# Kernel optimization log

Measured on AMD Instinct MI355X. Metric: run time of the kernel, lower is better.

The kernel has to match this reference:

```python
import jax, jax.numpy as jnp
import numpy as np
import math

B, S, FDIM, D_MODEL, N_SCALES = 8, 2048, 64, 512, 5

def _layer_norm(h, g, b, eps=1e-5):
    mu = h.mean(-1, keepdims=True)
    var = h.var(-1, keepdims=True)
    return (h - mu) * jax.lax.rsqrt(var + eps) * g + b

def setup_inputs() -> dict:
    key = jax.random.key(0)
    ks = jax.random.split(key, 12)
    sc = lambda fan_in: 1.0 / np.sqrt(fan_in)
    inp = {
        'x': jax.random.normal(ks[0], (B, S, FDIM), dtype=jnp.float32),
        # relative_positional_encoding: Linear(3, d_model)
        'w_rel': jax.random.uniform(ks[1], (D_MODEL, 3), minval=-sc(3), maxval=sc(3), dtype=jnp.float32),
        'b_rel': jnp.zeros((D_MODEL,), jnp.float32),
        # event_encoding_projection: Linear(feature_dim, d_model)
        'w_proj': jax.random.uniform(ks[2], (D_MODEL, FDIM), minval=-sc(FDIM), maxval=sc(FDIM), dtype=jnp.float32),
        'b_proj': jnp.zeros((D_MODEL,), jnp.float32),
        'g1': jnp.ones((D_MODEL,), jnp.float32), 'bt1': jnp.zeros((D_MODEL,), jnp.float32),
        'g2': jnp.ones((D_MODEL,), jnp.float32), 'bt2': jnp.zeros((D_MODEL,), jnp.float32),
        'alpha': jnp.asarray(0.5, jnp.float32),
        'sigma_w': jnp.ones((1,), jnp.float32),
        'wq': jax.random.uniform(ks[3], (FDIM, FDIM), minval=-sc(FDIM), maxval=sc(FDIM), dtype=jnp.float32),
        'bq': jnp.zeros((FDIM,), jnp.float32),
        'wk': jax.random.uniform(ks[4], (FDIM, FDIM), minval=-sc(FDIM), maxval=sc(FDIM), dtype=jnp.float32),
        'bk': jnp.zeros((FDIM,), jnp.float32),
        'scale_w': jax.nn.softplus(jax.random.normal(ks[5], (N_SCALES,), dtype=jnp.float32)),
    }
    return inp

def reference(x, w_rel, b_rel, w_proj, b_proj, g1, bt1, g2, bt2, alpha, sigma_w, wq, bq, wk, bk, scale_w):
    bsz, seq_len, fdim = x.shape
    # distances / energies are the first two physical feature channels
    distances = x[:, :, 0]
    energies = x[:, :, 1]
    dd_list, de_list, wd_list = [], [], []
    for scale in range(1, N_SCALES + 1):  # static small loop (clamp(5,3,15).round()=5)
        dd = distances[:, :-scale] - distances[:, scale:]
        de = energies[:, :-scale] - energies[:, scale:]
        wd = scale_w[scale - 1] * jnp.exp(-jnp.abs(dd) / (2.0 ** scale))
        pad = ((0, 0), (scale, 0))
        dd_list.append(jnp.pad(dd, pad))
        de_list.append(jnp.pad(de, pad))
        wd_list.append(jnp.pad(wd, pad))
    delta_distances = jnp.stack(dd_list, axis=-1)   # [B,S,n_scales]
    delta_energies = jnp.stack(de_list, axis=-1)
    weighted_distances = jnp.stack(wd_list, axis=-1)
    rel = jnp.stack([delta_distances, delta_energies, weighted_distances], axis=-1)  # [B,S,n_scales,3]
    rel_enc = (jnp.einsum('bsnt,dt->bsnd', rel, w_rel) + b_rel).sum(axis=2)  # [B,S,D]
    rel_enc = _layer_norm(rel_enc, g1, bt1)

    # hybrid similarity
    x_norm = x / jnp.maximum(jnp.linalg.norm(x, axis=-1, keepdims=True), 1e-12)
    cos_sim = (jnp.einsum('bsd,btd->bst', x_norm, x_norm) + 1.0) / 2.0
    # pairwise euclidean distance via gram trick (avoids B*S*S*d intermediate)
    sq = jnp.sum(x * x, axis=-1)                                  # [B,S]
    d2 = sq[:, :, None] + sq[:, None, :] - 2.0 * jnp.einsum('bsd,btd->bst', x, x)
    d2 = jnp.maximum(d2, 0.0)
    euclid = jnp.where(d2 > 0, jnp.sqrt(jnp.maximum(d2, 1e-12)), 0.0)
    mean_dist = euclid.mean()
    std_dist = jnp.std(euclid, ddof=1)
    dev = euclid - mean_dist
    euclid = jnp.where(jnp.abs(dev) > 2 * std_dist, jnp.sign(dev) * (2 * std_dist) + mean_dist, euclid)
    euclid = (euclid - euclid.min()) / (euclid.max() - euclid.min() + 1e-6)
    a = jax.nn.sigmoid(alpha)
    hybrid = a * cos_sim + (1 - a) * (1 - euclid)

    sigma = jax.nn.softplus(sigma_w) + 0.001          # [1]
    q = jnp.einsum('bsf,gf->bsg', x, wq) + bq
    k = jnp.einsum('bsf,gf->bsg', x, wk) + bk
    scores = jnp.einsum('bsg,btg->bst', q, k) / math.sqrt(fdim)
    weights = jax.nn.softmax(scores, axis=-1)
    E = weights * jnp.exp(-hybrid / (2.0 * sigma[0] ** 2))
    pe_event = jnp.einsum('bst,btf->bsf', E, x)
    pe_proj = jnp.einsum('bsf,df->bsd', pe_event, w_proj) + b_proj
    pe_proj = _layer_norm(pe_proj, g2, bt2)
    return rel_enc + pe_proj
```

## Files before the change

kernel.cpp:

```cpp
#include <hip/hip_runtime.h>
#include <math.h>

#define B_ 8
#define S_ 2048
#define F_ 64
#define D_ 512
#define NS_ 5
#define BS_ (B_*S_)
#define NTILE_ 528
#define NPART_ (NTILE_*B_)

typedef unsigned short u16;
typedef __attribute__((ext_vector_type(8))) short short8;
typedef __attribute__((ext_vector_type(4))) float f32x4;

#define WS_SQ    0
#define WS_REL   (BS_)
#define WS_PE    (4*BS_)
#define WS_STATS (68*BS_)
#define US_BASE_FLOATS (68*BS_ + 16)
#define US_XB 0
#define US_QB (BS_*64)
#define US_KB (2*BS_*64)
#define US_XT (3*BS_*64)

#define MFMA16(a,b,c) __builtin_amdgcn_mfma_f32_16x16x32_bf16(a,b,c,0,0,0)

__device__ __forceinline__ u16 f2bf(float f){
  unsigned u = __float_as_uint(f);
  return (u16)((u + 0x7FFFu + ((u>>16)&1u)) >> 16);
}
__device__ __forceinline__ int swz_phys(int row, int c){ return row*64 + (((c ^ (row & 15))) << 2); }

__global__ __launch_bounds__(256) void k1_prep(
    const float* __restrict__ x, const float* __restrict__ wq, const float* __restrict__ bq,
    const float* __restrict__ wk, const float* __restrict__ bk,
    const float* __restrict__ scale_w, float* __restrict__ ws, u16* __restrict__ usb)
{
  __shared__ __align__(16) float xl[16*68];
  __shared__ __align__(16) float wql[4096];
  __shared__ __align__(16) float wkl[4096];
  int tid = threadIdx.x, lane = tid & 63, wv = tid >> 6;
  int row0 = blockIdx.x * 16;
  {
    int r = tid >> 4, c = tid & 15;
    *(float4*)(xl + r*68 + c*4) = *(const float4*)(x + (size_t)(row0 + r)*F_ + c*4);
  }
  for (int i = 0; i < 4; ++i){
    int idx = tid + i*256;
    int g = idx >> 4, c = idx & 15;
    float4 v = *(const float4*)(wq + g*F_ + c*4);
    int pb = swz_phys(g, c);
    wql[pb]=v.x; wql[pb+1]=v.y; wql[pb+2]=v.z; wql[pb+3]=v.w;
    float4 u = *(const float4*)(wk + g*F_ + c*4);
    wkl[pb]=u.x; wkl[pb+1]=u.y; wkl[pb+2]=u.z; wkl[pb+3]=u.w;
  }
  __syncthreads();
  int g = lane;
  int swl = g & 15;
  float qa[4], ka[4];
  #pragma unroll
  for (int j=0;j<4;++j){ qa[j]=bq[g]; ka[j]=bk[g]; }
  #pragma unroll
  for (int c=0;c<16;++c){
    float4 wqv = *(const float4*)(wql + g*64 + ((c ^ swl)<<2));
    float4 wkv = *(const float4*)(wkl + g*64 + ((c ^ swl)<<2));
    #pragma unroll
    for (int j=0;j<4;++j){
      float4 xv = *(const float4*)(xl + (wv*4+j)*68 + c*4);
      qa[j] += xv.x*wqv.x + xv.y*wqv.y + xv.z*wqv.z + xv.w*wqv.w;
      ka[j] += xv.x*wkv.x + xv.y*wkv.y + xv.z*wkv.z + xv.w*wkv.w;
    }
  }
  #pragma unroll
  for (int j=0;j<4;++j){
    int rg = row0 + wv*4 + j;
    usb[US_QB + (size_t)rg*64 + g] = f2bf(qa[j]);
    usb[US_KB + (size_t)rg*64 + g] = f2bf(ka[j]);
  }
  #pragma unroll
  for (int j=0;j<4;++j){
    int r = wv*4 + j;
    float v = xl[r*68 + lane];
    float s = v*v;
    for (int o=32;o;o>>=1) s += __shfl_xor(s, o, 64);
    if (lane == 0) ws[WS_SQ + row0 + r] = s;
  }
  #pragma unroll
  for (int j=0;j<4;++j){
    int r = wv*4 + j;
    int rg = row0 + r;
    int b = rg >> 11, s_loc = rg & (S_-1);
    float d0 = xl[r*68 + 0], e0 = xl[r*68 + 1];
    float dd = 0.f, de = 0.f, wd = 0.f;
    int n = lane + 1;
    if (lane < NS_ && s_loc >= n){
      const float* xp = x + ((size_t)(b*S_ + s_loc - n))*F_;
      float dp_ = xp[0], ep = xp[1];
      dd = dp_ - d0;
      de = ep - e0;
      wd = scale_w[lane] * __expf(-fabsf(dd) * (1.0f/(float)(1<<n)));
    }
    for (int o=4;o;o>>=1){
      dd += __shfl_down(dd, o, 64);
      de += __shfl_down(de, o, 64);
      wd += __shfl_down(wd, o, 64);
    }
    if (lane == 0){
      ws[WS_REL + rg*3+0] = dd;
      ws[WS_REL + rg*3+1] = de;
      ws[WS_REL + rg*3+2] = wd;
    }
  }
  {
    int r = tid >> 4, cb = (tid & 15)*4;
    unsigned w0 = (unsigned)f2bf(xl[r*68+cb])   | ((unsigned)f2bf(xl[r*68+cb+1])<<16);
    unsigned w1 = (unsigned)f2bf(xl[r*68+cb+2]) | ((unsigned)f2bf(xl[r*68+cb+3])<<16);
    uint2 pk; pk.x = w0; pk.y = w1;
    *(uint2*)(usb + US_XB + (size_t)(row0+r)*64 + cb) = pk;
  }
  {
    int f = tid & 63, rg4 = (tid >> 6)*4;
    unsigned wa = (unsigned)f2bf(xl[(rg4+0)*68+f]) | ((unsigned)f2bf(xl[(rg4+1)*68+f])<<16);
    unsigned wb = (unsigned)f2bf(xl[(rg4+2)*68+f]) | ((unsigned)f2bf(xl[(rg4+3)*68+f])<<16);
    uint2 pk; pk.x = wa; pk.y = wb;
    int bb = row0 >> 11;
    int tloc = (row0 & (S_-1)) + rg4;
    *(uint2*)(usb + US_XT + (size_t)bb*64*2048 + (size_t)f*2048 + tloc) = pk;
  }
}

__global__ __launch_bounds__(256) void k2_stats(const u16* __restrict__ us, float* __restrict__ ws)
{
  __shared__ __align__(16) u16 Xls[4096];
  __shared__ float sqs_l[64], sqt_l[64];
  __shared__ float rsum[4], rss[4], rmn[4], rmx[4];
  int tid = threadIdx.x, lane = tid & 63, wv = tid >> 6;
  int lg = lane >> 4, lc = lane & 15;
  int b = blockIdx.y;
  int rem = blockIdx.x, i = 0;
  while (rem >= 32 - i){ rem -= 32 - i; ++i; }
  int j = i + rem;
  int s0 = i*64, t0 = j*64;
  size_t rb = (size_t)b * S_;
  const u16* xb = us + US_XB;
  #pragma unroll
  for (int p2=0;p2<2;++p2){
    int slot = tid + p2*256;
    int row = slot>>3, pc = slot&7, lcn = pc ^ (row&7);
    ((short8*)Xls)[slot] = *(const short8*)(xb + (rb + t0 + row)*64 + lcn*8);
  }
  if (tid < 64) sqs_l[tid] = ws[WS_SQ + rb + s0 + tid];
  else if (tid < 128) sqt_l[tid-64] = ws[WS_SQ + rb + t0 + (tid-64)];
  short8 a0 = *(const short8*)(xb + (rb + s0 + wv*16 + lc)*64 + lg*8);
  short8 a1 = *(const short8*)(xb + (rb + s0 + wv*16 + lc)*64 + 32 + lg*8);
  __syncthreads();
  f32x4 acc[4];
  #pragma unroll
  for (int t=0;t<4;++t){ acc[t][0]=0.f; acc[t][1]=0.f; acc[t][2]=0.f; acc[t][3]=0.f; }
  #pragma unroll
  for (int ts=0; ts<4; ++ts){
    int rowb = ts*16 + lc;
    int sw = rowb & 7;
    short8 b0 = *(const short8*)(Xls + rowb*64 + ((lg ^ sw)<<3));
    short8 b1 = *(const short8*)(Xls + rowb*64 + (((4+lg) ^ sw)<<3));
    acc[ts] = MFMA16(a0, b0, acc[ts]);
    acc[ts] = MFMA16(a1, b1, acc[ts]);
  }
  float sq_s[4];
  #pragma unroll
  for (int r=0;r<4;++r) sq_s[r] = sqs_l[wv*16 + lg*4 + r];
  float lsum=0.f, lss=0.f, lmn=3.4e38f, lmx=-3.4e38f;
  #pragma unroll
  for (int ts=0; ts<4; ++ts){
    float sqt = sqt_l[ts*16 + lc];
    #pragma unroll
    for (int r=0;r<4;++r){
      float gg = acc[ts][r];
      float d2 = sq_s[r] + sqt - 2.f*gg;
      d2 = fmaxf(d2, 0.f);
      float eu = d2 > 0.f ? sqrtf(d2) : 0.f;
      lsum += eu; lss += eu*eu;
      lmn = fminf(lmn, eu); lmx = fmaxf(lmx, eu);
    }
  }
  for (int o=32;o;o>>=1){
    lsum += __shfl_xor(lsum, o, 64);
    lss  += __shfl_xor(lss, o, 64);
    lmn = fminf(lmn, __shfl_xor(lmn, o, 64));
    lmx = fmaxf(lmx, __shfl_xor(lmx, o, 64));
  }
  if (lane == 0){ rsum[wv]=lsum; rss[wv]=lss; rmn[wv]=lmn; rmx[wv]=lmx; }
  __syncthreads();
  if (tid == 0){
    float bs=0.f, bss=0.f, bmn=3.4e38f, bmx=-3.4e38f;
    for (int w2=0;w2<4;++w2){ bs+=rsum[w2]; bss+=rss[w2]; bmn=fminf(bmn,rmn[w2]); bmx=fmaxf(bmx,rmx[w2]); }
    float wgt = (i==j) ? 1.f : 2.f;
    float* part = ws + WS_PE;
    int bid = blockIdx.y * NTILE_ + blockIdx.x;
    part[bid]           = bs*wgt;
    part[NPART_ + bid]  = bss*wgt;
    part[2*NPART_ + bid]= bmn;
    part[3*NPART_ + bid]= bmx;
  }
}

__global__ __launch_bounds__(256) void k3_fin(const float* __restrict__ alpha,
                                              const float* __restrict__ sigma_w, float* ws){
  __shared__ double ssm[256], sss[256];
  __shared__ float smn[256], smx[256];
  int tid = threadIdx.x;
  const float* part = ws + WS_PE;
  double s = 0.0, ss = 0.0;
  float mn = 3.4e38f, mx = -3.4e38f;
  for (int i2 = tid; i2 < NPART_; i2 += 256){
    s  += (double)part[i2];
    ss += (double)part[NPART_ + i2];
    mn = fminf(mn, part[2*NPART_ + i2]);
    mx = fmaxf(mx, part[3*NPART_ + i2]);
  }
  ssm[tid]=s; sss[tid]=ss; smn[tid]=mn; smx[tid]=mx;
  __syncthreads();
  for (int st = 128; st; st >>= 1){
    if (tid < st){
      ssm[tid] += ssm[tid+st];
      sss[tid] += sss[tid+st];
      smn[tid] = fminf(smn[tid], smn[tid+st]);
      smx[tid] = fmaxf(smx[tid], smx[tid+st]);
    }
    __syncthreads();
  }
  if (tid == 0){
    double N = (double)B_*S_*S_;
    double sum = ssm[0], sumsq = sss[0];
    double mean = sum/N;
    double var  = (sumsq - sum*sum/N) / (N - 1.0);
    float stdv = (float)sqrt(fmax(var, 0.0));
    float m = (float)mean;
    float lo = m - 2.f*stdv, hi = m + 2.f*stdv;
    float cmn = fminf(fmaxf(smn[0], lo), hi);
    float cmx = fminf(fmaxf(smx[0], lo), hi);
    float invr = 1.f/(cmx - cmn + 1e-6f);
    float a = 1.f/(1.f + expf(-alpha[0]));
    float swv = sigma_w[0];
    float sp = (swv > 20.f) ? swv : log1pf(expf(swv));
    float sg = sp + 0.001f;
    float efac = -0.5f/(sg*sg);
    float* p = ws + WS_STATS + 8;
    p[0]=lo; p[1]=hi; p[2]=cmn; p[3]=invr; p[4]=a; p[5]=1.f-a; p[6]=efac;
  }
}

__global__ __launch_bounds__(512) void k4_flash(const u16* __restrict__ us, float* __restrict__ ws)
{
  __shared__ __align__(16) u16 SMEM[16384];
  __shared__ float sqt_l[64], invt_l[64];
  __shared__ float zb[4][2][16];
  u16* Kls  = SMEM;
  u16* Xls  = SMEM + 4096;
  u16* XTls = SMEM + 8192;
  u16* elp  = SMEM + 12288;
  int tid = threadIdx.x, lane = tid & 63, wv = tid >> 6;
  int lg = lane >> 4, lc = lane & 15;
  int ssub = wv >> 1, th = wv & 1;
  int b = blockIdx.y;
  size_t rb = (size_t)b * S_;
  int s0 = blockIdx.x * 64;
  const u16* xb = us + US_XB;
  const u16* qb = us + US_QB;
  const u16* kb = us + US_KB;
  const u16* xt = us + US_XT + (size_t)b*64*2048;
  int srow = s0 + ssub*16 + lc;
  short8 qf0 = *(const short8*)(qb + (rb+srow)*64 + lg*8);
  short8 qf1 = *(const short8*)(qb + (rb+srow)*64 + 32 + lg*8);
  short8 xf0 = *(const short8*)(xb + (rb+srow)*64 + lg*8);
  short8 xf1 = *(const short8*)(xb + (rb+srow)*64 + 32 + lg*8);
  float sq_s[4], inv_s[4];
  #pragma unroll
  for (int r=0;r<4;++r){
    float s = ws[WS_SQ + rb + s0 + ssub*16 + lg*4 + r];
    sq_s[r] = s; inv_s[r] = 1.f / fmaxf(sqrtf(s), 1e-12f);
  }
  const float* prm = ws + WS_STATS + 8;
  float lo=prm[0], hi=prm[1], cmn=prm[2], invr=prm[3], a=prm[4], oma=prm[5], efac=prm[6];
  f32x4 pe[4];
  #pragma unroll
  for (int t=0;t<4;++t){ pe[t][0]=0.f; pe[t][1]=0.f; pe[t][2]=0.f; pe[t][3]=0.f; }
  float zrun[4];
  #pragma unroll
  for (int r=0;r<4;++r) zrun[r]=0.f;

  for (int t0 = 0; t0 < S_; t0 += 64){
    {
      int slot = tid;
      int row = slot>>3, pc = slot&7, lcn = pc ^ (row&7);
      ((short8*)Kls)[slot]  = *(const short8*)(kb + (rb + t0 + row)*64 + lcn*8);
      ((short8*)Xls)[slot]  = *(const short8*)(xb + (rb + t0 + row)*64 + lcn*8);
      ((short8*)XTls)[slot] = *(const short8*)(xt + (size_t)row*2048 + t0 + lcn*8);
    }
    if (tid < 64){
      float s = ws[WS_SQ + rb + t0 + tid];
      sqt_l[tid] = s;
      invt_l[tid] = 1.f / fmaxf(sqrtf(s), 1e-12f);
    }
    __syncthreads();
    f32x4 ga[2], sa[2];
    #pragma unroll
    for (int t=0;t<2;++t){ ga[t][0]=0.f; ga[t][1]=0.f; ga[t][2]=0.f; ga[t][3]=0.f;
                           sa[t][0]=0.f; sa[t][1]=0.f; sa[t][2]=0.f; sa[t][3]=0.f; }
    #pragma unroll
    for (int ts=0; ts<2; ++ts){
      int rowb = (2*th+ts)*16 + lc;
      int sw = rowb & 7;
      short8 bk0 = *(const short8*)(Kls + rowb*64 + ((lg ^ sw)<<3));
      short8 bx0 = *(const short8*)(Xls + rowb*64 + ((lg ^ sw)<<3));
      sa[ts] = MFMA16(qf0, bk0, sa[ts]);
      ga[ts] = MFMA16(xf0, bx0, ga[ts]);
      short8 bk1 = *(const short8*)(Kls + rowb*64 + (((4+lg) ^ sw)<<3));
      short8 bx1 = *(const short8*)(Xls + rowb*64 + (((4+lg) ^ sw)<<3));
      sa[ts] = MFMA16(qf1, bk1, sa[ts]);
      ga[ts] = MFMA16(xf1, bx1, ga[ts]);
    }
    #pragma unroll
    for (int ts=0; ts<2; ++ts){
      int col = (2*th+ts)*16 + lc;
      float sqt = sqt_l[col], invt = invt_l[col];
      #pragma unroll
      for (int r=0;r<4;++r){
        float gg = ga[ts][r];
        float cosv = (gg*inv_s[r]*invt + 1.f)*0.5f;
        float d2 = sq_s[r] + sqt - 2.f*gg;
        d2 = fmaxf(d2, 0.f);
        float eu = d2 > 0.f ? sqrtf(d2) : 0.f;
        eu = fminf(fmaxf(eu, lo), hi);
        float en = (eu - cmn)*invr;
        float hyb = a*cosv + oma*(1.f - en);
        float H = __expf(hyb*efac);
        float p = __expf(__builtin_fmaf(sa[ts][r], 0.125f, -8.f));
        zrun[r] += p;
        int rowl = lg*4 + r;
        int phys = rowl*64 + ((((col>>3) ^ (rowl&7)))<<3) + (col&7);
        elp[ssub*1024 + phys] = f2bf(p*H);
      }
    }
    {
      int swA = lc & 7;
      short8 Ae = *(const short8*)(elp + ssub*1024 + lc*64 + (((4*th + lg) ^ swA)<<3));
      #pragma unroll
      for (int fs=0; fs<4; ++fs){
        int rowf = fs*16 + lc;
        short8 Bx = *(const short8*)(XTls + rowf*64 + (((4*th + lg) ^ (rowf&7))<<3));
        pe[fs] = MFMA16(Ae, Bx, pe[fs]);
      }
    }
    __syncthreads();
  }
  #pragma unroll
  for (int r=0;r<4;++r){
    float z = zrun[r];
    z += __shfl_xor(z, 1, 64);
    z += __shfl_xor(z, 2, 64);
    z += __shfl_xor(z, 4, 64);
    z += __shfl_xor(z, 8, 64);
    if (lc == r) zb[ssub][th][lg*4+r] = z;
  }
  __syncthreads();
  float* tmp = (float*)SMEM;
  if (th == 1){
    #pragma unroll
    for (int fs=0; fs<4; ++fs)
      #pragma unroll
      for (int r=0;r<4;++r)
        tmp[ssub*1024 + (lg*4+r)*64 + fs*16 + lc] = pe[fs][r];
  }
  __syncthreads();
  if (th == 0){
    float zi[4];
    #pragma unroll
    for (int r=0;r<4;++r) zi[r] = 1.f / (zb[ssub][0][lg*4+r] + zb[ssub][1][lg*4+r]);
    #pragma unroll
    for (int fs=0; fs<4; ++fs)
      #pragma unroll
      for (int r=0;r<4;++r){
        float v = pe[fs][r] + tmp[ssub*1024 + (lg*4+r)*64 + fs*16 + lc];
        ws[WS_PE + (rb + s0 + ssub*16 + lg*4 + r)*64 + fs*16 + lc] = v * zi[r];
      }
  }
}

__global__ __launch_bounds__(256) void kpe_conv(const float* __restrict__ pef, u16* __restrict__ usb){
  size_t i = ((size_t)blockIdx.x*256 + threadIdx.x)*4;
  float4 v = *(const float4*)(pef + i);
  uint2 pk;
  pk.x = (unsigned)f2bf(v.x) | ((unsigned)f2bf(v.y)<<16);
  pk.y = (unsigned)f2bf(v.z) | ((unsigned)f2bf(v.w)<<16);
  *(uint2*)(usb + US_QB + i) = pk;
}

__global__ __launch_bounds__(256) void kw_conv(const float* __restrict__ wp, u16* __restrict__ usb){
  int i = (blockIdx.x*256 + threadIdx.x)*4;
  float4 v = *(const float4*)(wp + i);
  uint2 pk;
  pk.x = (unsigned)f2bf(v.x) | ((unsigned)f2bf(v.y)<<16);
  pk.y = (unsigned)f2bf(v.z) | ((unsigned)f2bf(v.w)<<16);
  *(uint2*)(usb + US_KB + i) = pk;
}

__global__ __launch_bounds__(256) void k5_final(
    const float* __restrict__ w_rel, const float* __restrict__ b_rel,
    const float* __restrict__ b_proj,
    const float* __restrict__ g1, const float* __restrict__ bt1,
    const float* __restrict__ g2, const float* __restrict__ bt2,
    const float* __restrict__ ws, const u16* __restrict__ usb, float* __restrict__ out)
{
  __shared__ __align__(16) float res[16*512];
  __shared__ float rsl[48];
  __shared__ float g1l[512], b1l[512], g2l[512], b2l[512], brl[512], wrl[1536];
  int tid = threadIdx.x, lane = tid & 63, wv = tid >> 6;
  int lg = lane >> 4, lc = lane & 15;
  int row0 = blockIdx.x * 16;
  const u16* peb = usb + US_QB;
  const u16* wb  = usb + US_KB;
  short8 a0 = *(const short8*)(peb + (size_t)(row0+lc)*64 + lg*8);
  short8 a1 = *(const short8*)(peb + (size_t)(row0+lc)*64 + 32 + lg*8);
  if (tid < 48) rsl[tid] = ws[WS_REL + row0*3 + tid];
  for (int i = tid; i < 512; i += 256){
    g1l[i]=g1[i]; b1l[i]=bt1[i]; g2l[i]=g2[i]; b2l[i]=bt2[i]; brl[i]=b_rel[i];
  }
  for (int i = tid; i < 1536; i += 256) wrl[i] = w_rel[i];
  int wc0 = wv*128;
  #pragma unroll
  for (int cg=0; cg<8; ++cg){
    int d = wc0 + cg*16 + lc;
    short8 b0 = *(const short8*)(wb + (size_t)d*64 + lg*8);
    short8 b1 = *(const short8*)(wb + (size_t)d*64 + 32 + lg*8);
    f32x4 acc = {0.f,0.f,0.f,0.f};
    acc = MFMA16(a0, b0, acc);
    acc = MFMA16(a1, b1, acc);
    float bp = b_proj[d];
    #pragma unroll
    for (int r=0;r<4;++r) res[(lg*4+r)*512 + d] = acc[r] + bp;
  }
  __syncthreads();
  #pragma unroll
  for (int j=0;j<4;++j){
    int r = wv*4 + j;
    int rg = row0 + r;
    float s1=0.f, q1=0.f;
    float vals[8];
    #pragma unroll
    for (int i=0;i<8;++i){ float v = res[r*512 + i*64 + lane]; vals[i]=v; s1+=v; q1+=v*v; }
    for (int o=32;o;o>>=1){ s1 += __shfl_xor(s1,o,64); q1 += __shfl_xor(q1,o,64); }
    float mu1 = s1*(1.f/512.f);
    float var1 = q1*(1.f/512.f) - mu1*mu1;
    float rsg1 = rsqrtf(fmaxf(var1, 0.f) + 1e-5f);
    float c0 = rsl[r*3+0], c1 = rsl[r*3+1], c2 = rsl[r*3+2];
    float rv[8]; float s2=0.f, q2=0.f;
    #pragma unroll
    for (int i=0;i<8;++i){
      int d = i*64 + lane;
      float v = c0*wrl[d*3+0] + c1*wrl[d*3+1] + c2*wrl[d*3+2] + 5.f*brl[d];
      rv[i]=v; s2+=v; q2+=v*v;
    }
    for (int o=32;o;o>>=1){ s2 += __shfl_xor(s2,o,64); q2 += __shfl_xor(q2,o,64); }
    float mu2 = s2*(1.f/512.f);
    float var2 = q2*(1.f/512.f) - mu2*mu2;
    float rsg2 = rsqrtf(fmaxf(var2, 0.f) + 1e-5f);
    #pragma unroll
    for (int i=0;i<8;++i){
      int d = i*64 + lane;
      float o1 = (vals[i]-mu1)*rsg1*g2l[d] + b2l[d];
      float o2 = (rv[i]-mu2)*rsg2*g1l[d] + b1l[d];
      out[(size_t)rg*512 + d] = o1 + o2;
    }
  }
}

extern "C" void kernel_launch(void* const* d_in, const int* in_sizes, int n_in,
                              void* d_out, int out_size, void* d_ws, size_t ws_size,
                              hipStream_t stream)
{
  const float* x      = (const float*)d_in[0];
  const float* w_rel  = (const float*)d_in[1];
  const float* b_rel  = (const float*)d_in[2];
  const float* w_proj = (const float*)d_in[3];
  const float* b_proj = (const float*)d_in[4];
  const float* g1     = (const float*)d_in[5];
  const float* bt1    = (const float*)d_in[6];
  const float* g2     = (const float*)d_in[7];
  const float* bt2    = (const float*)d_in[8];
  const float* alpha  = (const float*)d_in[9];
  const float* sigma_w= (const float*)d_in[10];
  const float* wq     = (const float*)d_in[11];
  const float* bq     = (const float*)d_in[12];
  const float* wk     = (const float*)d_in[13];
  const float* bk     = (const float*)d_in[14];
  const float* scale_w= (const float*)d_in[15];
  float* wsf = (float*)d_ws;
  u16*  usb = (u16*)(wsf + US_BASE_FLOATS);
  float* out = (float*)d_out;

  hipLaunchKernelGGL(k1_prep, dim3(BS_/16), dim3(256), 0, stream, x, wq, bq, wk, bk, scale_w, wsf, usb);
  hipLaunchKernelGGL(k2_stats, dim3(NTILE_, B_), dim3(256), 0, stream, usb, wsf);
  hipLaunchKernelGGL(k3_fin, dim3(1), dim3(256), 0, stream, alpha, sigma_w, wsf);
  hipLaunchKernelGGL(k4_flash, dim3(S_/64, B_), dim3(512), 0, stream, usb, wsf);
  hipLaunchKernelGGL(kpe_conv, dim3(BS_*64/1024), dim3(256), 0, stream, wsf + WS_PE, usb);
  hipLaunchKernelGGL(kw_conv, dim3(32), dim3(256), 0, stream, w_proj, usb);
  hipLaunchKernelGGL(k5_final, dim3(BS_/16), dim3(256), 0, stream,
                     w_rel, b_rel, b_proj, g1, bt1, g2, bt2, wsf, usb, out);
}
```

Baseline: 226.4 us.

## Fold hybrid-kernel constants, fuse bf16 conversions into producer kernels

Precomputes affine coefficients in k3_fin so the inner loop of k4_flash computes the exponent argument with a few FMAs and merges the two exponentials into exp(arg+s8), which cuts per-element ALU work. k4_flash now writes its normalized output directly as bf16 into the Q buffer. The w_proj bf16 conversion moves into k1_prep, so the kpe_conv and kw_conv launches and the fp32 PE round-trip go away. One risk is that k4 reads the Q buffer and overwrites it in the same launch. Different blocks touch different rows, which should keep this safe. The w_proj copy now lives in the freed WS_PE region.

Result: faster. 216.7 us (-4.3%).

```diff
diff --git a/kernel.cpp b/kernel.cpp
--- a/kernel.cpp
+++ b/kernel.cpp
@@ -17,6 +17,7 @@
 #define WS_SQ    0
 #define WS_REL   (BS_)
 #define WS_PE    (4*BS_)
+#define WS_WPB   (WS_PE + 20480)
 #define WS_STATS (68*BS_)
 #define US_BASE_FLOATS (68*BS_ + 16)
 #define US_XB 0
@@ -35,7 +36,8 @@
 __global__ __launch_bounds__(256) void k1_prep(
     const float* __restrict__ x, const float* __restrict__ wq, const float* __restrict__ bq,
     const float* __restrict__ wk, const float* __restrict__ bk,
-    const float* __restrict__ scale_w, float* __restrict__ ws, u16* __restrict__ usb)
+    const float* __restrict__ scale_w, const float* __restrict__ wp,
+    float* __restrict__ ws, u16* __restrict__ usb, u16* __restrict__ wpb)
 {
   __shared__ __align__(16) float xl[16*68];
   __shared__ __align__(16) float wql[4096];
@@ -54,6 +56,14 @@
     wql[pb]=v.x; wql[pb+1]=v.y; wql[pb+2]=v.z; wql[pb+3]=v.w;
     float4 u = *(const float4*)(wk + g*F_ + c*4);
     wkl[pb]=u.x; wkl[pb+1]=u.y; wkl[pb+2]=u.z; wkl[pb+3]=u.w;
+  }
+  if (blockIdx.x < 32){
+    int i2 = (blockIdx.x*256 + tid)*4;
+    float4 v = *(const float4*)(wp + i2);
+    uint2 pk2;
+    pk2.x = (unsigned)f2bf(v.x) | ((unsigned)f2bf(v.y)<<16);
+    pk2.y = (unsigned)f2bf(v.z) | ((unsigned)f2bf(v.w)<<16);
+    *(uint2*)(wpb + i2) = pk2;
   }
   __syncthreads();
   int g = lane;
@@ -242,16 +252,21 @@
     float cmx = fminf(fmaxf(smx[0], lo), hi);
     float invr = 1.f/(cmx - cmn + 1e-6f);
     float a = 1.f/(1.f + expf(-alpha[0]));
+    float oma = 1.f - a;
     float swv = sigma_w[0];
     float sp = (swv > 20.f) ? swv : log1pf(expf(swv));
     float sg = sp + 0.001f;
     float efac = -0.5f/(sg*sg);
+    float cg = efac*a*0.5f;
+    float ce = -efac*oma*invr;
+    float cc = efac*(a*0.5f + oma + oma*invr*cmn);
     float* p = ws + WS_STATS + 8;
-    p[0]=lo; p[1]=hi; p[2]=cmn; p[3]=invr; p[4]=a; p[5]=1.f-a; p[6]=efac;
-  }
-}
-
-__global__ __launch_bounds__(512) void k4_flash(const u16* __restrict__ us, float* __restrict__ ws)
+    p[0]=lo; p[1]=hi; p[2]=cg; p[3]=ce; p[4]=cc;
+  }
+}
+
+__global__ __launch_bounds__(512) void k4_flash(const u16* __restrict__ us,
+                                                float* __restrict__ ws, u16* qout)
 {
   __shared__ __align__(16) u16 SMEM[16384];
   __shared__ float sqt_l[64], invt_l[64];
@@ -275,14 +290,15 @@
   short8 qf1 = *(const short8*)(qb + (rb+srow)*64 + 32 + lg*8);
   short8 xf0 = *(const short8*)(xb + (rb+srow)*64 + lg*8);
   short8 xf1 = *(const short8*)(xb + (rb+srow)*64 + 32 + lg*8);
-  float sq_s[4], inv_s[4];
+  const float* prm = ws + WS_STATS + 8;
+  float lo=prm[0], hi=prm[1], cg=prm[2], ce=prm[3], cc=prm[4];
+  float sq_s[4], cgis[4];
   #pragma unroll
   for (int r=0;r<4;++r){
     float s = ws[WS_SQ + rb + s0 + ssub*16 + lg*4 + r];
-    sq_s[r] = s; inv_s[r] = 1.f / fmaxf(sqrtf(s), 1e-12f);
-  }
-  const float* prm = ws + WS_STATS + 8;
-  float lo=prm[0], hi=prm[1], cmn=prm[2], invr=prm[3], a=prm[4], oma=prm[5], efac=prm[6];
+    sq_s[r] = s;
+    cgis[r] = cg / fmaxf(sqrtf(s), 1e-12f);
+  }
   f32x4 pe[4];
   #pragma unroll
   for (int t=0;t<4;++t){ pe[t][0]=0.f; pe[t][1]=0.f; pe[t][2]=0.f; pe[t][3]=0.f; }
@@ -328,19 +344,17 @@
       #pragma unroll
       for (int r=0;r<4;++r){
         float gg = ga[ts][r];
-        float cosv = (gg*inv_s[r]*invt + 1.f)*0.5f;
-        float d2 = sq_s[r] + sqt - 2.f*gg;
-        d2 = fmaxf(d2, 0.f);
-        float eu = d2 > 0.f ? sqrtf(d2) : 0.f;
-        eu = fminf(fmaxf(eu, lo), hi);
-        float en = (eu - cmn)*invr;
-        float hyb = a*cosv + oma*(1.f - en);
-        float H = __expf(hyb*efac);
-        float p = __expf(__builtin_fmaf(sa[ts][r], 0.125f, -8.f));
+        float d2 = fmaxf(__builtin_fmaf(-2.f, gg, sq_s[r] + sqt), 0.f);
+        float eu = fminf(fmaxf(sqrtf(d2), lo), hi);
+        float arg = __builtin_fmaf(cgis[r]*invt, gg, cc);
+        arg = __builtin_fmaf(ce, eu, arg);
+        float s8 = __builtin_fmaf(sa[ts][r], 0.125f, -8.f);
+        float p = __expf(s8);
+        float pH = __expf(arg + s8);
         zrun[r] += p;
         int rowl = lg*4 + r;
         int phys = rowl*64 + ((((col>>3) ^ (rowl&7)))<<3) + (col&7);
-        elp[ssub*1024 + phys] = f2bf(p*H);
+        elp[ssub*1024 + phys] = f2bf(pH);
       }
     }
     {
@@ -383,27 +397,9 @@
       #pragma unroll
       for (int r=0;r<4;++r){
         float v = pe[fs][r] + tmp[ssub*1024 + (lg*4+r)*64 + fs*16 + lc];
-        ws[WS_PE + (rb + s0 + ssub*16 + lg*4 + r)*64 + fs*16 + lc] = v * zi[r];
+        qout[US_QB + (rb + s0 + ssub*16 + lg*4 + r)*64 + fs*16 + lc] = f2bf(v * zi[r]);
       }
   }
-}
-
-__global__ __launch_bounds__(256) void kpe_conv(const float* __restrict__ pef, u16* __restrict__ usb){
-  size_t i = ((size_t)blockIdx.x*256 + threadIdx.x)*4;
-  float4 v = *(const float4*)(pef + i);
-  uint2 pk;
-  pk.x = (unsigned)f2bf(v.x) | ((unsigned)f2bf(v.y)<<16);
-  pk.y = (unsigned)f2bf(v.z) | ((unsigned)f2bf(v.w)<<16);
-  *(uint2*)(usb + US_QB + i) = pk;
-}
-
-__global__ __launch_bounds__(256) void kw_conv(const float* __restrict__ wp, u16* __restrict__ usb){
-  int i = (blockIdx.x*256 + threadIdx.x)*4;
-  float4 v = *(const float4*)(wp + i);
-  uint2 pk;
-  pk.x = (unsigned)f2bf(v.x) | ((unsigned)f2bf(v.y)<<16);
-  pk.y = (unsigned)f2bf(v.z) | ((unsigned)f2bf(v.w)<<16);
-  *(uint2*)(usb + US_KB + i) = pk;
 }
 
 __global__ __launch_bounds__(256) void k5_final(
@@ -411,7 +407,8 @@
     const float* __restrict__ b_proj,
     const float* __restrict__ g1, const float* __restrict__ bt1,
     const float* __restrict__ g2, const float* __restrict__ bt2,
-    const float* __restrict__ ws, const u16* __restrict__ usb, float* __restrict__ out)
+    const float* __restrict__ ws, const u16* __restrict__ usb,
+    const u16* __restrict__ wpb, float* __restrict__ out)
 {
   __shared__ __align__(16) float res[16*512];
   __shared__ float rsl[48];
@@ -420,7 +417,6 @@
   int lg = lane >> 4, lc = lane & 15;
   int row0 = blockIdx.x * 16;
   const u16* peb = usb + US_QB;
-  const u16* wb  = usb + US_KB;
   short8 a0 = *(const short8*)(peb + (size_t)(row0+lc)*64 + lg*8);
   short8 a1 = *(const short8*)(peb + (size_t)(row0+lc)*64 + 32 + lg*8);
   if (tid < 48) rsl[tid] = ws[WS_REL + row0*3 + tid];
@@ -432,8 +428,8 @@
   #pragma unroll
   for (int cg=0; cg<8; ++cg){
     int d = wc0 + cg*16 + lc;
-    short8 b0 = *(const short8*)(wb + (size_t)d*64 + lg*8);
-    short8 b1 = *(const short8*)(wb + (size_t)d*64 + 32 + lg*8);
+    short8 b0 = *(const short8*)(wpb + (size_t)d*64 + lg*8);
+    short8 b1 = *(const short8*)(wpb + (size_t)d*64 + 32 + lg*8);
     f32x4 acc = {0.f,0.f,0.f,0.f};
     acc = MFMA16(a0, b0, acc);
     acc = MFMA16(a1, b1, acc);
@@ -498,14 +494,14 @@
   const float* scale_w= (const float*)d_in[15];
   float* wsf = (float*)d_ws;
   u16*  usb = (u16*)(wsf + US_BASE_FLOATS);
+  u16*  wpb = (u16*)(wsf + WS_WPB);
   float* out = (float*)d_out;
 
-  hipLaunchKernelGGL(k1_prep, dim3(BS_/16), dim3(256), 0, stream, x, wq, bq, wk, bk, scale_w, wsf, usb);
+  hipLaunchKernelGGL(k1_prep, dim3(BS_/16), dim3(256), 0, stream,
+                     x, wq, bq, wk, bk, scale_w, w_proj, wsf, usb, wpb);
   hipLaunchKernelGGL(k2_stats, dim3(NTILE_, B_), dim3(256), 0, stream, usb, wsf);
   hipLaunchKernelGGL(k3_fin, dim3(1), dim3(256), 0, stream, alpha, sigma_w, wsf);
-  hipLaunchKernelGGL(k4_flash, dim3(S_/64, B_), dim3(512), 0, stream, usb, wsf);
-  hipLaunchKernelGGL(kpe_conv, dim3(BS_*64/1024), dim3(256), 0, stream, wsf + WS_PE, usb);
-  hipLaunchKernelGGL(kw_conv, dim3(32), dim3(256), 0, stream, w_proj, usb);
+  hipLaunchKernelGGL(k4_flash, dim3(S_/64, B_), dim3(512), 0, stream, usb, wsf, usb);
   hipLaunchKernelGGL(k5_final, dim3(BS_/16), dim3(256), 0, stream,
-                     w_rel, b_rel, b_proj, g1, bt1, g2, bt2, wsf, usb, out);
-}
+                     w_rel, b_rel, b_proj, g1, bt1, g2, bt2, wsf, usb, wpb, out);
+}
```
